# Kernel tuning notes

Measured on AMD Instinct MI355X. Metric: run time of the kernel, lower is better.

Reference implementation:

```python
import jax, jax.numpy as jnp
import numpy as np

# Map flattened lm index (l<=3, 16 components) -> l value, used to expand
# the per-l tp_weights [E,4,C] to per-lm weights [E,16,C].
L_OF_LM = jnp.array([0, 1, 1, 1, 2, 2, 2, 2, 2, 3, 3, 3, 3, 3, 3, 3], dtype=jnp.int32)

NNODES = 25000
NEDGES = 400000
NCHAN = 64


def setup_inputs() -> dict:
    key = jax.random.key(0)
    k1, k2, k3, k4 = jax.random.split(key, 4)
    node_feats = jax.random.normal(k1, (NNODES, NCHAN), dtype=jnp.float32)
    edge_attrs = jax.random.normal(k2, (NEDGES, 16), dtype=jnp.float32)
    tp_weights = jax.random.normal(k3, (NEDGES, 4, NCHAN), dtype=jnp.float32)
    receiver_list = jnp.sort(
        jax.random.randint(k4, (NEDGES,), 0, NNODES, dtype=jnp.int64)
    )
    return {
        "node_feats": node_feats,
        "edge_attrs": edge_attrs,
        "tp_weights": tp_weights,
        "receiver_list": receiver_list,
        "nnodes": NNODES,
    }


def reference(node_feats, edge_attrs, tp_weights, receiver_list, nnodes):
    # Gather per-edge node features: [E, C]
    feats = node_feats[receiver_list]
    # Expand per-l weights to per-lm weights: [E, 16, C]
    w_lm = tp_weights[:, L_OF_LM, :]
    # Invariant tensor product message: [E, 16, C]
    msg = edge_attrs[:, :, None] * w_lm * feats[:, None, :]
    # Scatter-add messages to receiver nodes: [nnodes, 16, C]
    return jax.ops.segment_sum(msg, receiver_list, num_segments=nnodes)
```

## Files before the change

kernel.cpp:

```cpp
#include <hip/hip_runtime.h>


#define FMA16(EA_OFF, W0, W1, W2, W3)                                         \
    acc[0]  += ea[EA_OFF + 0]  * W0;                                          \
    acc[1]  += ea[EA_OFF + 1]  * W1;                                          \
    acc[2]  += ea[EA_OFF + 2]  * W1;                                          \
    acc[3]  += ea[EA_OFF + 3]  * W1;                                          \
    acc[4]  += ea[EA_OFF + 4]  * W2;                                          \
    acc[5]  += ea[EA_OFF + 5]  * W2;                                          \
    acc[6]  += ea[EA_OFF + 6]  * W2;                                          \
    acc[7]  += ea[EA_OFF + 7]  * W2;                                          \
    acc[8]  += ea[EA_OFF + 8]  * W2;                                          \
    acc[9]  += ea[EA_OFF + 9]  * W3;                                          \
    acc[10] += ea[EA_OFF + 10] * W3;                                          \
    acc[11] += ea[EA_OFF + 11] * W3;                                          \
    acc[12] += ea[EA_OFF + 12] * W3;                                          \
    acc[13] += ea[EA_OFF + 13] * W3;                                          \
    acc[14] += ea[EA_OFF + 14] * W3;                                          \
    acc[15] += ea[EA_OFF + 15] * W3;

__global__ __launch_bounds__(256) void bounds_kernel(
    const int* __restrict__ recv, int nedges, int nnodes,
    int* __restrict__ off)
{
    const int n = blockIdx.x * blockDim.x + threadIdx.x;
    if (n > nnodes) return;
    int lo = 0, hi = nedges;
    while (lo < hi) { int mid = (lo + hi) >> 1; if (recv[mid] < n) lo = mid + 1; else hi = mid; }
    off[n] = lo;
}

__global__ __launch_bounds__(256) void imp_tp_main(
    const float* __restrict__ node_feats,
    const float* __restrict__ edge_attrs,
    const float* __restrict__ tp_weights,
    const int*   __restrict__ off,
    int nnodes,
    float* __restrict__ out)
{
    const int wave = (blockIdx.x * blockDim.x + threadIdx.x) >> 6;
    const int lane = threadIdx.x & 63;
    if (wave >= nnodes) return;
    const int n = wave;

    const int start = __builtin_amdgcn_readfirstlane(off[n]);
    const int end   = __builtin_amdgcn_readfirstlane(off[n + 1]);

    const float nf = node_feats[(size_t)n * 64 + lane];

    float acc[16];
    #pragma unroll
    for (int i = 0; i < 16; ++i) acc[i] = 0.f;

    int e = start;
    for (; e + 2 <= end; e += 2) {
        const float* wp = tp_weights + (size_t)e * 256 + lane;
        const float a0 = wp[0];
        const float a1 = wp[64];
        const float a2 = wp[128];
        const float a3 = wp[192];
        const float b0 = wp[256];
        const float b1 = wp[320];
        const float b2 = wp[384];
        const float b3 = wp[448];
        const float* eap = edge_attrs + (size_t)e * 16;
        float ea[32];
        #pragma unroll
        for (int i = 0; i < 32; ++i) ea[i] = eap[i];

        FMA16(0,  a0, a1, a2, a3)
        FMA16(16, b0, b1, b2, b3)
    }
    if (e < end) {
        const float* wp = tp_weights + (size_t)e * 256 + lane;
        const float a0 = wp[0];
        const float a1 = wp[64];
        const float a2 = wp[128];
        const float a3 = wp[192];
        const float* eap = edge_attrs + (size_t)e * 16;
        float ea[16];
        #pragma unroll
        for (int i = 0; i < 16; ++i) ea[i] = eap[i];
        FMA16(0, a0, a1, a2, a3)
    }

    float* o = out + (size_t)n * 1024 + lane;
    #pragma unroll
    for (int lm = 0; lm < 16; ++lm) o[lm * 64] = acc[lm] * nf;
}

__global__ __launch_bounds__(256) void imp_tp_fallback(
    const float* __restrict__ node_feats,
    const float* __restrict__ edge_attrs,
    const float* __restrict__ tp_weights,
    const int*   __restrict__ recv,
    int nnodes, int nedges,
    float* __restrict__ out)
{
    const int wave = (blockIdx.x * blockDim.x + threadIdx.x) >> 6;
    const int lane = threadIdx.x & 63;
    if (wave >= nnodes) return;
    const int n = wave;

    int lo = 0, hi = nedges;
    while (lo < hi) { int mid = (lo + hi) >> 1; if (recv[mid] < n) lo = mid + 1; else hi = mid; }
    const int start = lo;
    hi = nedges;
    while (lo < hi) { int mid = (lo + hi) >> 1; if (recv[mid] < n + 1) lo = mid + 1; else hi = mid; }
    const int end = lo;

    float acc[16];
    #pragma unroll
    for (int i = 0; i < 16; ++i) acc[i] = 0.f;

    for (int e = start; e < end; ++e) {
        const float4* ea4 = reinterpret_cast<const float4*>(edge_attrs + (size_t)e * 16);
        const float4 ea0 = ea4[0];
        const float4 ea1 = ea4[1];
        const float4 ea2 = ea4[2];
        const float4 ea3 = ea4[3];
        const float* w = tp_weights + (size_t)e * 256 + lane;
        const float w0 = w[0];
        const float w1 = w[64];
        const float w2 = w[128];
        const float w3 = w[192];

        acc[0]  += ea0.x * w0;
        acc[1]  += ea0.y * w1;
        acc[2]  += ea0.z * w1;
        acc[3]  += ea0.w * w1;
        acc[4]  += ea1.x * w2;
        acc[5]  += ea1.y * w2;
        acc[6]  += ea1.z * w2;
        acc[7]  += ea1.w * w2;
        acc[8]  += ea2.x * w2;
        acc[9]  += ea2.y * w3;
        acc[10] += ea2.z * w3;
        acc[11] += ea2.w * w3;
        acc[12] += ea3.x * w3;
        acc[13] += ea3.y * w3;
        acc[14] += ea3.z * w3;
        acc[15] += ea3.w * w3;
    }

    const float nf = node_feats[(size_t)n * 64 + lane];
    float* o = out + (size_t)n * 1024 + lane;
    #pragma unroll
    for (int lm = 0; lm < 16; ++lm) o[lm * 64] = acc[lm] * nf;
}

extern "C" void kernel_launch(void* const* d_in, const int* in_sizes, int n_in,
                              void* d_out, int out_size, void* d_ws, size_t ws_size,
                              hipStream_t stream) {
    const float* node_feats = (const float*)d_in[0];
    const float* edge_attrs = (const float*)d_in[1];
    const float* tp_weights = (const float*)d_in[2];
    const int*   recv       = (const int*)d_in[3];
    float* out = (float*)d_out;

    const int nnodes = in_sizes[0] / 64;
    const int nedges = in_sizes[1] / 16;

    const int threads = 256;
    const int blocks = (nnodes * 64 + threads - 1) / threads;

    if (ws_size >= (size_t)(nnodes + 1) * sizeof(int)) {
        int* off = (int*)d_ws;
        const int bthreads = 256;
        const int bblocks = (nnodes + 1 + bthreads - 1) / bthreads;
        bounds_kernel<<<bblocks, bthreads, 0, stream>>>(recv, nedges, nnodes, off);
        imp_tp_main<<<blocks, threads, 0, stream>>>(
            node_feats, edge_attrs, tp_weights, off, nnodes, out);
    } else {
        imp_tp_fallback<<<blocks, threads, 0, stream>>>(
            node_feats, edge_attrs, tp_weights, recv, nnodes, nedges, out);
    }
}
```

Measured before the change: 123.8 us.

## Split wave into two edge halves with packed float2 FMAs and shuffle reduction

```diff
diff --git a/kernel.cpp b/kernel.cpp
--- a/kernel.cpp
+++ b/kernel.cpp
@@ -1,23 +1,28 @@
 #include <hip/hip_runtime.h>
 
 
-#define FMA16(EA_OFF, W0, W1, W2, W3)                                         \
-    acc[0]  += ea[EA_OFF + 0]  * W0;                                          \
-    acc[1]  += ea[EA_OFF + 1]  * W1;                                          \
-    acc[2]  += ea[EA_OFF + 2]  * W1;                                          \
-    acc[3]  += ea[EA_OFF + 3]  * W1;                                          \
-    acc[4]  += ea[EA_OFF + 4]  * W2;                                          \
-    acc[5]  += ea[EA_OFF + 5]  * W2;                                          \
-    acc[6]  += ea[EA_OFF + 6]  * W2;                                          \
-    acc[7]  += ea[EA_OFF + 7]  * W2;                                          \
-    acc[8]  += ea[EA_OFF + 8]  * W2;                                          \
-    acc[9]  += ea[EA_OFF + 9]  * W3;                                          \
-    acc[10] += ea[EA_OFF + 10] * W3;                                          \
-    acc[11] += ea[EA_OFF + 11] * W3;                                          \
-    acc[12] += ea[EA_OFF + 12] * W3;                                          \
-    acc[13] += ea[EA_OFF + 13] * W3;                                          \
-    acc[14] += ea[EA_OFF + 14] * W3;                                          \
-    acc[15] += ea[EA_OFF + 15] * W3;
+typedef float v2f __attribute__((ext_vector_type(2)));
+typedef float v4f __attribute__((ext_vector_type(4)));
+
+#define PFMA(A, EAS, W) A = __builtin_elementwise_fma((v2f){(EAS), (EAS)}, (W), (A))
+
+#define FMA16_V2(EA0, EA1, EA2, EA3, W0, W1, W2, W3)                          \
+    PFMA(acc[0],  (EA0).x, W0);                                               \
+    PFMA(acc[1],  (EA0).y, W1);                                               \
+    PFMA(acc[2],  (EA0).z, W1);                                               \
+    PFMA(acc[3],  (EA0).w, W1);                                               \
+    PFMA(acc[4],  (EA1).x, W2);                                               \
+    PFMA(acc[5],  (EA1).y, W2);                                               \
+    PFMA(acc[6],  (EA1).z, W2);                                               \
+    PFMA(acc[7],  (EA1).w, W2);                                               \
+    PFMA(acc[8],  (EA2).x, W2);                                               \
+    PFMA(acc[9],  (EA2).y, W3);                                               \
+    PFMA(acc[10], (EA2).z, W3);                                               \
+    PFMA(acc[11], (EA2).w, W3);                                               \
+    PFMA(acc[12], (EA3).x, W3);                                               \
+    PFMA(acc[13], (EA3).y, W3);                                               \
+    PFMA(acc[14], (EA3).z, W3);                                               \
+    PFMA(acc[15], (EA3).w, W3);
 
 __global__ __launch_bounds__(256) void bounds_kernel(
     const int* __restrict__ recv, int nedges, int nnodes,
@@ -42,51 +47,64 @@
     const int lane = threadIdx.x & 63;
     if (wave >= nnodes) return;
     const int n = wave;
+    const int k = lane & 31;
+    const int h = lane >> 5;
 
     const int start = __builtin_amdgcn_readfirstlane(off[n]);
     const int end   = __builtin_amdgcn_readfirstlane(off[n + 1]);
 
-    const float nf = node_feats[(size_t)n * 64 + lane];
-
-    float acc[16];
+    v2f acc[16];
     #pragma unroll
-    for (int i = 0; i < 16; ++i) acc[i] = 0.f;
+    for (int i = 0; i < 16; ++i) acc[i] = (v2f)0.f;
 
     int e = start;
     for (; e + 2 <= end; e += 2) {
-        const float* wp = tp_weights + (size_t)e * 256 + lane;
-        const float a0 = wp[0];
-        const float a1 = wp[64];
-        const float a2 = wp[128];
-        const float a3 = wp[192];
-        const float b0 = wp[256];
-        const float b1 = wp[320];
-        const float b2 = wp[384];
-        const float b3 = wp[448];
-        const float* eap = edge_attrs + (size_t)e * 16;
-        float ea[32];
-        #pragma unroll
-        for (int i = 0; i < 32; ++i) ea[i] = eap[i];
+        const int eidx = e + h;
+        const float* wp = tp_weights + (size_t)eidx * 256 + 2 * k;
+        const v2f w0 = *(const v2f*)(wp);
+        const v2f w1 = *(const v2f*)(wp + 64);
+        const v2f w2 = *(const v2f*)(wp + 128);
+        const v2f w3 = *(const v2f*)(wp + 192);
+        const float* eap = edge_attrs + (size_t)eidx * 16;
+        const v4f ea0 = *(const v4f*)(eap);
+        const v4f ea1 = *(const v4f*)(eap + 4);
+        const v4f ea2 = *(const v4f*)(eap + 8);
+        const v4f ea3 = *(const v4f*)(eap + 12);
 
-        FMA16(0,  a0, a1, a2, a3)
-        FMA16(16, b0, b1, b2, b3)
+        FMA16_V2(ea0, ea1, ea2, ea3, w0, w1, w2, w3)
     }
     if (e < end) {
-        const float* wp = tp_weights + (size_t)e * 256 + lane;
-        const float a0 = wp[0];
-        const float a1 = wp[64];
-        const float a2 = wp[128];
-        const float a3 = wp[192];
+        const float* wp = tp_weights + (size_t)e * 256 + 2 * k;
+        const v2f w0 = *(const v2f*)(wp);
+        const v2f w1 = *(const v2f*)(wp + 64);
+        const v2f w2 = *(const v2f*)(wp + 128);
+        const v2f w3 = *(const v2f*)(wp + 192);
         const float* eap = edge_attrs + (size_t)e * 16;
-        float ea[16];
-        #pragma unroll
-        for (int i = 0; i < 16; ++i) ea[i] = eap[i];
-        FMA16(0, a0, a1, a2, a3)
+        const v4f ea0 = *(const v4f*)(eap);
+        const v4f ea1 = *(const v4f*)(eap + 4);
+        const v4f ea2 = *(const v4f*)(eap + 8);
+        const v4f ea3 = *(const v4f*)(eap + 12);
+        if (h == 0) {
+            FMA16_V2(ea0, ea1, ea2, ea3, w0, w1, w2, w3)
+        }
     }
 
-    float* o = out + (size_t)n * 1024 + lane;
     #pragma unroll
-    for (int lm = 0; lm < 16; ++lm) o[lm * 64] = acc[lm] * nf;
+    for (int i = 0; i < 16; ++i) {
+        acc[i].x += __shfl_xor(acc[i].x, 32);
+        acc[i].y += __shfl_xor(acc[i].y, 32);
+    }
+
+    const v2f nf = *(const v2f*)(node_feats + (size_t)n * 64 + 2 * k);
+
+    float* obase = out + (size_t)n * 1024 + (size_t)(h * 8) * 64 + 2 * k;
+    #pragma unroll
+    for (int j = 0; j < 8; ++j) {
+        const v2f lo = acc[j];
+        const v2f hi = acc[j + 8];
+        const v2f v = h ? hi : lo;
+        *(v2f*)(obase + j * 64) = v * nf;
+    }
 }
 
 __global__ __launch_bounds__(256) void imp_tp_fallback(
```

New measurement: 132.7 us. 1.07x slower.
